# Kernel tuning notes

Hardware: AMD Instinct MI355X
Metric: run time of the kernel (lower is better)

The kernel has to match this reference:

```python
import jax, jax.numpy as jnp
import numpy as np

B, S, K, D, F, H, L, MLP = 8, 1024, 11, 512, 768, 8, 4, 2048
HD = D // H
LN_EPS = 1e-5
QK_EPS = 1e-6
SCALE = HD ** -0.5
W_STD = 0.02


def _ln(x, g, b):
    m = x.mean(-1, keepdims=True)
    v = ((x - m) ** 2).mean(-1, keepdims=True)
    return (x - m) / jnp.sqrt(v + LN_EPS) * g + b


def _lin(x, w, b):  # torch Linear: y = x @ W.T + b, W is [out, in]
    return jnp.einsum('...i,oi->...o', x, w) + b


def _heads(x):  # [b, t, D] -> [b, H, t, HD]
    b, t, _ = x.shape
    return x.reshape(b, t, H, HD).transpose(0, 2, 1, 3)


def _l2norm(x):  # F.normalize(dim=-1, eps=QK_EPS)
    n = jnp.sqrt((x * x).sum(-1, keepdims=True))
    return x / jnp.maximum(n, QK_EPS)


def _mha(xq, xkv, qw, qb, kw, kb, vw, vb, ow, ob, mask):
    q = _l2norm(_heads(_lin(xq, qw, qb)))
    k = _l2norm(_heads(_lin(xkv, kw, kb)))
    v = _heads(_lin(xkv, vw, vb))
    s = jnp.einsum('bhtd,bhsd->bhts', q, k) * SCALE
    if mask is not None:
        s = jnp.where(mask, jnp.finfo(s.dtype).min, s)
    a = jax.nn.softmax(s, axis=-1)
    c = jnp.einsum('bhts,bhsd->bhtd', a, v)
    c = c.transpose(0, 2, 1, 3).reshape(xq.shape[0], xq.shape[1], D)
    return _lin(c, ow, ob), a


def setup_inputs() -> dict:
    key = jax.random.key(0)
    ks = jax.random.split(key, 16)
    inp = {
        'features': jax.random.normal(ks[0], (B, S, F), jnp.float32),
        'slots': jax.random.normal(ks[1], (B, K, D), jnp.float32),
        'tok_w': jax.random.normal(ks[2], (D, F), jnp.float32) * W_STD,
        'tok_b': jnp.zeros((D,), jnp.float32),
        'slot_g': jnp.ones((D,), jnp.float32),
        'slot_b': jnp.zeros((D,), jnp.float32),
        'ln1_g': jnp.ones((L, D), jnp.float32),
        'ln1_b': jnp.zeros((L, D), jnp.float32),
        'ln2_g': jnp.ones((L, D), jnp.float32),
        'ln2_b': jnp.zeros((L, D), jnp.float32),
        'ln3_g': jnp.ones((L, D), jnp.float32),
        'ln3_b': jnp.zeros((L, D), jnp.float32),
    }
    names = ['sa_qw', 'sa_kw', 'sa_vw', 'sa_ow', 'ca_qw', 'ca_kw', 'ca_vw', 'ca_ow']
    for i, n in enumerate(names):
        inp[n] = jax.random.normal(ks[3 + i], (L, D, D), jnp.float32) * W_STD
        inp[n[:-1] + 'b'] = jnp.zeros((L, D), jnp.float32)
    inp['ffn_w1'] = jax.random.normal(ks[11], (L, MLP, D), jnp.float32) * W_STD
    inp['ffn_b1'] = jnp.zeros((L, MLP), jnp.float32)
    inp['ffn_w2'] = jax.random.normal(ks[12], (L, D, MLP), jnp.float32) * W_STD
    inp['ffn_b2'] = jnp.zeros((L, D), jnp.float32)
    return inp


def reference(features, slots, tok_w, tok_b, slot_g, slot_b,
              ln1_g, ln1_b, sa_qw, sa_qb, sa_kw, sa_kb, sa_vw, sa_vb, sa_ow, sa_ob,
              ln2_g, ln2_b, ca_qw, ca_qb, ca_kw, ca_kb, ca_vw, ca_vb, ca_ow, ca_ob,
              ln3_g, ln3_b, ffn_w1, ffn_b1, ffn_w2, ffn_b2):
    tokens = _lin(features, tok_w, tok_b)            # [B, S, D]
    slots_n = _ln(slots, slot_g, slot_b)             # [B, K, D]
    causal = jnp.triu(jnp.ones((S, S), bool), k=1)[None, None]  # True = masked
    cross_sum = jnp.zeros((B, S, K), tokens.dtype)
    for l in range(L):
        h = _ln(tokens, ln1_g[l], ln1_b[l])
        sa, _ = _mha(h, h, sa_qw[l], sa_qb[l], sa_kw[l], sa_kb[l],
                     sa_vw[l], sa_vb[l], sa_ow[l], sa_ob[l], causal)
        tokens = tokens + sa
        h = _ln(tokens, ln2_g[l], ln2_b[l])
        ca, w = _mha(h, slots_n, ca_qw[l], ca_qb[l], ca_kw[l], ca_kb[l],
                     ca_vw[l], ca_vb[l], ca_ow[l], ca_ob[l], None)
        tokens = tokens + ca
        cross_sum = cross_sum + w.mean(axis=1)       # avg over heads
        h = _ln(tokens, ln3_g[l], ln3_b[l])
        h = jax.nn.gelu(_lin(h, ffn_w1[l], ffn_b1[l]), approximate=False)
        tokens = tokens + _lin(h, ffn_w2[l], ffn_b2[l])
    masks = cross_sum / L                            # [B, S, K] avg over blocks
    return tokens, masks
```

## Files before the change

### kernel.cpp

```cpp
#include <hip/hip_runtime.h>
#include <math.h>

#define DEV __device__ __forceinline__

typedef __attribute__((ext_vector_type(4))) float f32x4;
typedef __attribute__((ext_vector_type(8))) short bf16x8;

DEV ushort f2bf(float x) {
  unsigned u = __float_as_uint(x);
  u = (u + 0x7FFFu + ((u >> 16) & 1u)) >> 16;
  return (ushort)u;
}

DEV float bf2f(ushort u) { return __uint_as_float(((unsigned)u) << 16); }

DEV ushort4 cvt4(float4 f) {
  ushort4 u;
  u.x = f2bf(f.x); u.y = f2bf(f.y); u.z = f2bf(f.z); u.w = f2bf(f.w);
  return u;
}

DEV float gelu_exact(float x) {
  return 0.5f * x * (1.0f + erff(x * 0.70710678118654752f));
}

DEV void async16(const void* g, void* l) {
  __builtin_amdgcn_global_load_lds((const __attribute__((address_space(1))) void*)g,
                                   (__attribute__((address_space(3))) void*)l, 16, 0, 0);
}

__global__ void prep_all(const float* __restrict__ features, const float* __restrict__ tok_w,
                         const float* __restrict__ sa_qw, const float* __restrict__ sa_kw,
                         const float* __restrict__ sa_vw, const float* __restrict__ sa_ow,
                         const float* __restrict__ ca_qw, const float* __restrict__ ca_kw,
                         const float* __restrict__ ca_vw, const float* __restrict__ ca_ow,
                         const float* __restrict__ ffn_w1, const float* __restrict__ ffn_w2,
                         const float* __restrict__ sa_qb, const float* __restrict__ sa_kb,
                         const float* __restrict__ sa_vb, const float* __restrict__ ca_kb,
                         const float* __restrict__ ca_vb,
                         ushort* __restrict__ featbf, ushort* __restrict__ tokwbf,
                         ushort* __restrict__ saowbf, ushort* __restrict__ caqwbf,
                         ushort* __restrict__ caowbf, ushort* __restrict__ w1bf,
                         ushort* __restrict__ w2bf, ushort* __restrict__ qkvwbf,
                         ushort* __restrict__ kvwbf, float* __restrict__ qkvb,
                         float* __restrict__ kvb) {
  long i = (long)blockIdx.x * 256 + threadIdx.x;
  if (i < 1572864) { ((ushort4*)featbf)[i] = cvt4(((const float4*)features)[i]); return; }
  i -= 1572864;
  if (i < 98304) { ((ushort4*)tokwbf)[i] = cvt4(((const float4*)tok_w)[i]); return; }
  i -= 98304;
  if (i < 262144) { ((ushort4*)saowbf)[i] = cvt4(((const float4*)sa_ow)[i]); return; }
  i -= 262144;
  if (i < 262144) { ((ushort4*)caqwbf)[i] = cvt4(((const float4*)ca_qw)[i]); return; }
  i -= 262144;
  if (i < 262144) { ((ushort4*)caowbf)[i] = cvt4(((const float4*)ca_ow)[i]); return; }
  i -= 262144;
  if (i < 1048576) { ((ushort4*)w1bf)[i] = cvt4(((const float4*)ffn_w1)[i]); return; }
  i -= 1048576;
  if (i < 1048576) { ((ushort4*)w2bf)[i] = cvt4(((const float4*)ffn_w2)[i]); return; }
  i -= 1048576;
  if (i < 786432) {
    const long o = i * 4;
    const int layer = (int)(o / 786432), r = (int)(o % 786432);
    const int sel = r / 262144, off = r % 262144;
    const float* s = (sel == 0 ? sa_qw : sel == 1 ? sa_kw : sa_vw) + (size_t)layer * 262144 + off;
    ((ushort4*)qkvwbf)[i] = cvt4(*(const float4*)s);
    return;
  }
  i -= 786432;
  if (i < 524288) {
    const long o = i * 4;
    const int layer = (int)(o / 524288), r = (int)(o % 524288);
    const int sel = r / 262144, off = r % 262144;
    const float* s = (sel == 0 ? ca_kw : ca_vw) + (size_t)layer * 262144 + off;
    ((ushort4*)kvwbf)[i] = cvt4(*(const float4*)s);
    return;
  }
  i -= 524288;
  if (i < 1536) {
    const long o = i * 4;
    const int layer = (int)(o / 1536), r = (int)(o % 1536);
    const int sel = r / 512, off = r % 512;
    const float* s = (sel == 0 ? sa_qb : sel == 1 ? sa_kb : sa_vb) + layer * 512 + off;
    ((float4*)qkvb)[i] = *(const float4*)s;
    return;
  }
  i -= 1536;
  if (i < 1024) {
    const long o = i * 4;
    const int layer = (int)(o / 1024), r = (int)(o % 1024);
    const int sel = r / 512, off = r % 512;
    const float* s = (sel == 0 ? ca_kb : ca_vb) + layer * 512 + off;
    ((float4*)kvb)[i] = *(const float4*)s;
  }
}

template <int EPI>
__launch_bounds__(256, 2)
__global__ void gemm_bt(const ushort* __restrict__ A, const ushort* __restrict__ W,
                        const float* __restrict__ bias, float* __restrict__ Yf,
                        ushort* __restrict__ Ybf, int M, int N, int K) {
  __shared__ ushort As[128 * 32];
  __shared__ ushort Bs[128 * 32];
  const int tid  = threadIdx.x;
  const int lane = tid & 63;
  const int wave = tid >> 6;
  const int wr = wave >> 1, wc = wave & 1;
  const int m0 = blockIdx.x * 128, n0 = blockIdx.y * 128;
  const int q = lane >> 4, ln = lane & 15;
  const int srow = lane >> 2;
  const int scol = (lane & 3) * 8;

  f32x4 acc[4][4] = {};

  const ushort* gA = A + (size_t)(m0 + wave * 32 + srow) * K + scol;
  const ushort* gB = W + (size_t)(n0 + wave * 32 + srow) * K + scol;
  ushort* lA = &As[(wave * 32) * 32];
  ushort* lB = &Bs[(wave * 32) * 32];

  for (int k0 = 0; k0 < K; k0 += 32) {
    async16(gA + k0, lA);
    async16(gA + k0 + (size_t)16 * K, lA + 16 * 32);
    async16(gB + k0, lB);
    async16(gB + k0 + (size_t)16 * K, lB + 16 * 32);
    __syncthreads();
    bf16x8 af[4], bfr[4];
#pragma unroll
    for (int t = 0; t < 4; ++t)
      af[t] = *(const bf16x8*)&As[(wr * 64 + t * 16 + ln) * 32 + q * 8];
#pragma unroll
    for (int t = 0; t < 4; ++t)
      bfr[t] = *(const bf16x8*)&Bs[(wc * 64 + t * 16 + ln) * 32 + q * 8];
#pragma unroll
    for (int mt = 0; mt < 4; ++mt)
#pragma unroll
      for (int nt = 0; nt < 4; ++nt)
        acc[mt][nt] = __builtin_amdgcn_mfma_f32_16x16x32_bf16(af[mt], bfr[nt], acc[mt][nt], 0, 0, 0);
    __syncthreads();
  }

  if (EPI >= 4) {
    const int chunk = (n0 + wc * 64) >> 9;
    const bool donorm = (EPI == 5 && chunk == 0) || (EPI == 6 && chunk < 2);
    const bool doscale = (EPI == 6 && chunk == 0);
#pragma unroll
    for (int mt = 0; mt < 4; ++mt) {
      const int gm = m0 + wr * 64 + mt * 16 + q * 4;
      float val[4][4];
#pragma unroll
      for (int nt = 0; nt < 4; ++nt) {
        const float bi = bias[n0 + wc * 64 + nt * 16 + ln];
#pragma unroll
        for (int r = 0; r < 4; ++r) val[nt][r] = acc[mt][nt][r] + bi;
      }
#pragma unroll
      for (int r = 0; r < 4; ++r) {
        float mult = 1.f;
        if (donorm) {
          float ss = val[0][r]*val[0][r] + val[1][r]*val[1][r] +
                     val[2][r]*val[2][r] + val[3][r]*val[3][r];
          ss += __shfl_xor(ss, 1);
          ss += __shfl_xor(ss, 2);
          ss += __shfl_xor(ss, 4);
          ss += __shfl_xor(ss, 8);
          mult = 1.f / fmaxf(sqrtf(ss), 1e-6f);
          if (doscale) mult *= 0.125f;
        }
#pragma unroll
        for (int nt = 0; nt < 4; ++nt) {
          const int gn = n0 + wc * 64 + nt * 16 + ln;
          Ybf[(size_t)(gm + r) * N + gn] = f2bf(val[nt][r] * mult);
        }
      }
    }
  } else {
#pragma unroll
    for (int mt = 0; mt < 4; ++mt) {
      const int gm = m0 + wr * 64 + mt * 16 + q * 4;
#pragma unroll
      for (int nt = 0; nt < 4; ++nt) {
        const int gn = n0 + wc * 64 + nt * 16 + ln;
        const float bi = bias[gn];
#pragma unroll
        for (int r = 0; r < 4; ++r) {
          const float val = acc[mt][nt][r] + bi;
          const size_t idx = (size_t)(gm + r) * N + gn;
          if (EPI == 0)      Yf[idx] = val;
          else if (EPI == 1) Yf[idx] += val;
          else               Ybf[idx] = f2bf(gelu_exact(val));
        }
      }
    }
  }
}

template <int EPI>
__launch_bounds__(256, 4)
__global__ void gemm_bt64(const ushort* __restrict__ A, const ushort* __restrict__ W,
                          const float* __restrict__ bias, float* __restrict__ Yf,
                          ushort* __restrict__ Ybf, int M, int N, int K) {
  __shared__ ushort As[64 * 32];
  __shared__ ushort Bs[64 * 32];
  __shared__ float red[2][32][2];
  const int tid = threadIdx.x, lane = tid & 63, wave = tid >> 6;
  const int wr = wave >> 1, wc = wave & 1;
  const int m0 = blockIdx.x * 64, n0 = blockIdx.y * 64;
  const int q = lane >> 4, ln = lane & 15;

  f32x4 acc[2][2] = {};
  const ushort* gA = A + (size_t)(m0 + wave * 16 + (lane >> 2)) * K + (lane & 3) * 8;
  const ushort* gB = W + (size_t)(n0 + wave * 16 + (lane >> 2)) * K + (lane & 3) * 8;
  ushort* lA = &As[wave * 16 * 32];
  ushort* lB = &Bs[wave * 16 * 32];

  for (int k0 = 0; k0 < K; k0 += 32) {
    async16(gA + k0, lA);
    async16(gB + k0, lB);
    __syncthreads();
    bf16x8 af[2], bfr[2];
#pragma unroll
    for (int t = 0; t < 2; ++t)
      af[t] = *(const bf16x8*)&As[(wr * 32 + t * 16 + ln) * 32 + q * 8];
#pragma unroll
    for (int t = 0; t < 2; ++t)
      bfr[t] = *(const bf16x8*)&Bs[(wc * 32 + t * 16 + ln) * 32 + q * 8];
#pragma unroll
    for (int mt = 0; mt < 2; ++mt)
#pragma unroll
      for (int nt = 0; nt < 2; ++nt)
        acc[mt][nt] = __builtin_amdgcn_mfma_f32_16x16x32_bf16(af[mt], bfr[nt], acc[mt][nt], 0, 0, 0);
    __syncthreads();
  }

  if (EPI == 4) {
    float val[2][2][4];
#pragma unroll
    for (int mt = 0; mt < 2; ++mt)
#pragma unroll
      for (int nt = 0; nt < 2; ++nt) {
        const float bi = bias[n0 + wc * 32 + nt * 16 + ln];
#pragma unroll
        for (int r = 0; r < 4; ++r) val[mt][nt][r] = acc[mt][nt][r] + bi;
      }
#pragma unroll
    for (int mt = 0; mt < 2; ++mt)
#pragma unroll
      for (int r = 0; r < 4; ++r) {
        float ss = val[mt][0][r]*val[mt][0][r] + val[mt][1][r]*val[mt][1][r];
        ss += __shfl_xor(ss, 1);
        ss += __shfl_xor(ss, 2);
        ss += __shfl_xor(ss, 4);
        ss += __shfl_xor(ss, 8);
        if (ln == 0) red[wr][mt * 16 + q * 4 + r][wc] = ss;
      }
    __syncthreads();
#pragma unroll
    for (int mt = 0; mt < 2; ++mt) {
      const int gm = m0 + wr * 32 + mt * 16 + q * 4;
#pragma unroll
      for (int r = 0; r < 4; ++r) {
        const float tot = red[wr][mt * 16 + q * 4 + r][0] + red[wr][mt * 16 + q * 4 + r][1];
        const float inv = 0.125f / fmaxf(sqrtf(tot), 1e-6f);
#pragma unroll
        for (int nt = 0; nt < 2; ++nt) {
          const int gn = n0 + wc * 32 + nt * 16 + ln;
          Ybf[(size_t)(gm + r) * N + gn] = f2bf(val[mt][nt][r] * inv);
        }
      }
    }
  } else {
#pragma unroll
    for (int mt = 0; mt < 2; ++mt) {
      const int gm = m0 + wr * 32 + mt * 16 + q * 4;
#pragma unroll
      for (int nt = 0; nt < 2; ++nt) {
        const int gn = n0 + wc * 32 + nt * 16 + ln;
        const float bi = bias[gn];
#pragma unroll
        for (int r = 0; r < 4; ++r) {
          const float val = acc[mt][nt][r] + bi;
          const size_t idx = (size_t)(gm + r) * N + gn;
          if (EPI == 0) Yf[idx] = val;
          else          Yf[idx] += val;
        }
      }
    }
  }
}

template <int BF>
__launch_bounds__(256)
__global__ void ln512(const float* __restrict__ X, const float* __restrict__ G,
                      const float* __restrict__ Bb, void* __restrict__ Yv, int rows) {
  const int lane = threadIdx.x & 63;
  const int wave = threadIdx.x >> 6;
  const int row = blockIdx.x * 4 + wave;
  if (row >= rows) return;
  const float* x = X + (size_t)row * 512 + lane * 8;
  float4 v0 = *(const float4*)x;
  float4 v1 = *(const float4*)(x + 4);
  float s = v0.x + v0.y + v0.z + v0.w + v1.x + v1.y + v1.z + v1.w;
#pragma unroll
  for (int off = 32; off; off >>= 1) s += __shfl_xor(s, off);
  const float mean = s * (1.f / 512.f);
  float d[8] = {v0.x - mean, v0.y - mean, v0.z - mean, v0.w - mean,
                v1.x - mean, v1.y - mean, v1.z - mean, v1.w - mean};
  float ss = d[0]*d[0] + d[1]*d[1] + d[2]*d[2] + d[3]*d[3] +
             d[4]*d[4] + d[5]*d[5] + d[6]*d[6] + d[7]*d[7];
#pragma unroll
  for (int off = 32; off; off >>= 1) ss += __shfl_xor(ss, off);
  const float rstd = rsqrtf(ss * (1.f / 512.f) + 1e-5f);
  const float* gp = G + lane * 8;
  const float* bp = Bb + lane * 8;
  float4 g0 = *(const float4*)gp, g1 = *(const float4*)(gp + 4);
  float4 b0 = *(const float4*)bp, b1 = *(const float4*)(bp + 4);
  float y[8];
  y[0] = d[0]*rstd*g0.x + b0.x; y[1] = d[1]*rstd*g0.y + b0.y;
  y[2] = d[2]*rstd*g0.z + b0.z; y[3] = d[3]*rstd*g0.w + b0.w;
  y[4] = d[4]*rstd*g1.x + b1.x; y[5] = d[5]*rstd*g1.y + b1.y;
  y[6] = d[6]*rstd*g1.z + b1.z; y[7] = d[7]*rstd*g1.w + b1.w;
  if (BF) {
    ushort* o = (ushort*)Yv + (size_t)row * 512 + lane * 8;
    ushort4 u0, u1;
    u0.x = f2bf(y[0]); u0.y = f2bf(y[1]); u0.z = f2bf(y[2]); u0.w = f2bf(y[3]);
    u1.x = f2bf(y[4]); u1.y = f2bf(y[5]); u1.z = f2bf(y[6]); u1.w = f2bf(y[7]);
    *(ushort4*)o = u0; *(ushort4*)(o + 4) = u1;
  } else {
    float* o = (float*)Yv + (size_t)row * 512 + lane * 8;
    *(float4*)o = make_float4(y[0], y[1], y[2], y[3]);
    *(float4*)(o + 4) = make_float4(y[4], y[5], y[6], y[7]);
  }
}

__launch_bounds__(256, 2)
__global__ void attn_self_mfma(const ushort* __restrict__ QKV, ushort* __restrict__ O) {
  constexpr int LDK = 72;
  __shared__ ushort Ks[64 * LDK];
  __shared__ ushort Vt[64 * LDK];
  __shared__ ushort Ps[4][32 * LDK];
  ushort* Qstage = &Ps[0][0];
  const int bi = blockIdx.x;
  const int half = bi >> 8, j = bi & 255;
  const int qt = half ? 7 - (j >> 5) : (j >> 5);
  const int bh = (half << 5) | (j & 31);
  const int b = bh >> 3, h = bh & 7;
  const size_t base = (size_t)b * 1024 * 1536 + h * 64;
  const int tid = threadIdx.x, lane = tid & 63, wave = tid >> 6;
  const int quad = lane >> 4, ln = lane & 15;

  const int kr = tid >> 2, kc0 = (tid & 3) * 16;
  const ushort* kbase = QKV + base + 512 + (size_t)kr * 1536 + kc0;
  const int vk = (tid & 31) * 2, vd0 = (tid >> 5) * 8;
  const ushort* vbase = QKV + base + 1024 + (size_t)vk * 1536 + vd0;

#pragma unroll
  for (int it = 0; it < 4; ++it) {
    const int idx = tid + 256 * it;
    const int r = idx >> 3, c = (idx & 7) * 8;
    *(uint4*)&Qstage[r * LDK + c] =
        *(const uint4*)(QKV + base + (size_t)(qt * 128 + r) * 1536 + c);
  }
  uint4 kreg0 = *(const uint4*)kbase;
  uint4 kreg1 = *(const uint4*)(kbase + 8);
  uint4 vreg0 = *(const uint4*)vbase;
  uint4 vreg1 = *(const uint4*)(vbase + 1536);
  __syncthreads();
  bf16x8 qf[2][2];
#pragma unroll
  for (int mt = 0; mt < 2; ++mt)
#pragma unroll
    for (int kc = 0; kc < 2; ++kc)
      qf[mt][kc] = *(const bf16x8*)&Qstage[(wave * 32 + mt * 16 + ln) * LDK + kc * 32 + quad * 8];

  float l_r[2][4] = {};
  f32x4 o_acc[2][4] = {};

  const int ktmax = 2 * qt + 1;
  for (int kt = 0; kt <= ktmax; ++kt) {
    __syncthreads();
    *(uint4*)&Ks[kr * LDK + kc0]     = kreg0;
    *(uint4*)&Ks[kr * LDK + kc0 + 8] = kreg1;
    {
      const ushort* ua = (const ushort*)&vreg0;
      const ushort* ub = (const ushort*)&vreg1;
#pragma unroll
      for (int jj = 0; jj < 8; ++jj)
        *(unsigned*)&Vt[(vd0 + jj) * LDK + vk] = (unsigned)ua[jj] | ((unsigned)ub[jj] << 16);
    }
    __syncthreads();
    if (kt < ktmax) {
      const size_t nb = (size_t)(kt + 1) * 64 * 1536;
      kreg0 = *(const uint4*)(kbase + nb);
      kreg1 = *(const uint4*)(kbase + nb + 8);
      vreg0 = *(const uint4*)(vbase + nb);
      vreg1 = *(const uint4*)(vbase + nb + 1536);
    }

    bf16x8 kf[4][2];
#pragma unroll
    for (int kb = 0; kb < 4; ++kb)
#pragma unroll
      for (int kc = 0; kc < 2; ++kc)
        kf[kb][kc] = *(const bf16x8*)&Ks[(kb * 16 + ln) * LDK + kc * 32 + quad * 8];
    f32x4 s[2][4] = {};
#pragma unroll
    for (int mt = 0; mt < 2; ++mt)
#pragma unroll
      for (int kb = 0; kb < 4; ++kb) {
        s[mt][kb] = __builtin_amdgcn_mfma_f32_16x16x32_bf16(qf[mt][0], kf[kb][0], s[mt][kb], 0, 0, 0);
        s[mt][kb] = __builtin_amdgcn_mfma_f32_16x16x32_bf16(qf[mt][1], kf[kb][1], s[mt][kb], 0, 0, 0);
      }

    const bool diag = (kt >= 2 * qt);
#pragma unroll
    for (int mt = 0; mt < 2; ++mt) {
      const int qrow0 = qt * 128 + wave * 32 + mt * 16 + quad * 4;
#pragma unroll
      for (int kb = 0; kb < 4; ++kb) {
        const int kcol = kt * 64 + kb * 16 + ln;
#pragma unroll
        for (int r = 0; r < 4; ++r) {
          float p = __expf(s[mt][kb][r]);
          if (diag && kcol > qrow0 + r) p = 0.f;
          l_r[mt][r] += p;
          Ps[wave][(mt * 16 + quad * 4 + r) * LDK + kb * 16 + ln] = f2bf(p);
        }
      }
    }
    __builtin_amdgcn_wave_barrier();

    bf16x8 pf[2][2];
#pragma unroll
    for (int mt = 0; mt < 2; ++mt)
#pragma unroll
      for (int kc = 0; kc < 2; ++kc)
        pf[mt][kc] = *(const bf16x8*)&Ps[wave][(mt * 16 + ln) * LDK + kc * 32 + quad * 8];
#pragma unroll
    for (int db = 0; db < 4; ++db) {
      bf16x8 vf0 = *(const bf16x8*)&Vt[(db * 16 + ln) * LDK + quad * 8];
      bf16x8 vf1 = *(const bf16x8*)&Vt[(db * 16 + ln) * LDK + 32 + quad * 8];
#pragma unroll
      for (int mt = 0; mt < 2; ++mt) {
        o_acc[mt][db] = __builtin_amdgcn_mfma_f32_16x16x32_bf16(pf[mt][0], vf0, o_acc[mt][db], 0, 0, 0);
        o_acc[mt][db] = __builtin_amdgcn_mfma_f32_16x16x32_bf16(pf[mt][1], vf1, o_acc[mt][db], 0, 0, 0);
      }
    }
  }

  const size_t obase = (size_t)b * 1024 * 512 + h * 64;
#pragma unroll
  for (int mt = 0; mt < 2; ++mt) {
    const int qrow0 = qt * 128 + wave * 32 + mt * 16 + quad * 4;
#pragma unroll
    for (int r = 0; r < 4; ++r) {
      float l = l_r[mt][r];
      l += __shfl_xor(l, 1);
      l += __shfl_xor(l, 2);
      l += __shfl_xor(l, 4);
      l += __shfl_xor(l, 8);
      const float inv = 1.f / l;
      ushort* dst = O + obase + (size_t)(qrow0 + r) * 512;
#pragma unroll
      for (int db = 0; db < 4; ++db)
        dst[db * 16 + ln] = f2bf(o_acc[mt][db][r] * inv);
    }
  }
}

__launch_bounds__(128)
__global__ void attn_cross(const ushort* __restrict__ Q, const ushort* __restrict__ KV,
                           ushort* __restrict__ Obf, float* __restrict__ mask_out) {
  const int rt = blockIdx.x;
  const int bh = blockIdx.y;
  const int b = bh >> 3, h = bh & 7;
  const int tid = threadIdx.x;
  __shared__ float Qs[128][65];
  __shared__ float Kcs[11][64];
  __shared__ float Vcs[11][64];
  const size_t base = ((size_t)(b * 1024)) * 512 + h * 64;

  for (int i = tid; i < 704; i += 128) {
    const int k = i >> 6, d = i & 63;
    Kcs[k][d] = bf2f(KV[((size_t)(b * 11 + k)) * 1024 + h * 64 + d]);
    Vcs[k][d] = bf2f(KV[((size_t)(b * 11 + k)) * 1024 + 512 + h * 64 + d]);
  }
#pragma unroll
  for (int it = 0; it < 8; ++it) {
    const int idx = tid + 128 * it;
    const int r = idx >> 3, c = (idx & 7) * 8;
    uint4 t = *(const uint4*)(Q + base + (size_t)(rt * 128 + r) * 512 + c);
    const ushort* u = (const ushort*)&t;
#pragma unroll
    for (int jj = 0; jj < 8; ++jj) Qs[r][c + jj] = bf2f(u[jj]);
  }
  __syncthreads();

  float s[11] = {};
  for (int d = 0; d < 64; ++d) {
    const float qv = Qs[tid][d];
#pragma unroll
    for (int k = 0; k < 11; ++k) s[k] += qv * Kcs[k][d];
  }
  float l = 0.f;
#pragma unroll
  for (int k = 0; k < 11; ++k) { s[k] = __expf(s[k]); l += s[k]; }
  const float inv = 1.f / l;
#pragma unroll
  for (int k = 0; k < 11; ++k) s[k] *= inv;

  const int qrow = rt * 128 + tid;
  float* mo = mask_out + ((size_t)(b * 1024 + qrow)) * 11;
#pragma unroll
  for (int k = 0; k < 11; ++k) atomicAdd(mo + k, s[k] * 0.03125f);

  ushort* dst = Obf + base + (size_t)qrow * 512;
#pragma unroll
  for (int d0 = 0; d0 < 64; d0 += 8) {
    ushort o8[8];
#pragma unroll
    for (int jj = 0; jj < 8; ++jj) {
      float acc = 0.f;
#pragma unroll
      for (int k = 0; k < 11; ++k) acc += s[k] * Vcs[k][d0 + jj];
      o8[jj] = f2bf(acc);
    }
    *(uint4*)(dst + d0) = *(const uint4*)o8;
  }
}

extern "C" void kernel_launch(void* const* d_in, const int* in_sizes, int n_in,
                              void* d_out, int out_size, void* d_ws, size_t ws_size,
                              hipStream_t stream) {
  const float* features = (const float*)d_in[0];
  const float* slots    = (const float*)d_in[1];
  const float* tok_w    = (const float*)d_in[2];
  const float* tok_b    = (const float*)d_in[3];
  const float* slot_g   = (const float*)d_in[4];
  const float* slot_b   = (const float*)d_in[5];
  const float* ln1_g    = (const float*)d_in[6];
  const float* ln1_b    = (const float*)d_in[7];
  const float* ln2_g    = (const float*)d_in[8];
  const float* ln2_b    = (const float*)d_in[9];
  const float* ln3_g    = (const float*)d_in[10];
  const float* ln3_b    = (const float*)d_in[11];
  const float* sa_qw = (const float*)d_in[12]; const float* sa_qb = (const float*)d_in[13];
  const float* sa_kw = (const float*)d_in[14]; const float* sa_kb = (const float*)d_in[15];
  const float* sa_vw = (const float*)d_in[16]; const float* sa_vb = (const float*)d_in[17];
  const float* sa_ow = (const float*)d_in[18]; const float* sa_ob = (const float*)d_in[19];
  const float* ca_qw = (const float*)d_in[20]; const float* ca_qb = (const float*)d_in[21];
  const float* ca_kw = (const float*)d_in[22]; const float* ca_kb = (const float*)d_in[23];
  const float* ca_vw = (const float*)d_in[24]; const float* ca_vb = (const float*)d_in[25];
  const float* ca_ow = (const float*)d_in[26]; const float* ca_ob = (const float*)d_in[27];
  const float* ffn_w1 = (const float*)d_in[28]; const float* ffn_b1 = (const float*)d_in[29];
  const float* ffn_w2 = (const float*)d_in[30]; const float* ffn_b2 = (const float*)d_in[31];

  float* tokens = (float*)d_out;
  float* masks  = (float*)d_out + 4194304;

  char* wp = (char*)d_ws;
  size_t off = 0;
  auto carve = [&](size_t bytes) -> void* {
    void* p = wp + off;
    off = (off + bytes + 255) & ~(size_t)255;
    return p;
  };
  ushort* hbf     = (ushort*)carve(8192ull * 512 * 2);
  ushort* qkvbf   = (ushort*)carve(8192ull * 1536 * 2);
  ushort* qbf     = (ushort*)carve(8192ull * 512 * 2);
  ushort* cbf     = (ushort*)carve(8192ull * 512 * 2);
  ushort* hidbf   = (ushort*)carve(8192ull * 2048 * 2);
  ushort* slotsn  = (ushort*)carve(128ull * 512 * 2);
  ushort* kvc     = (ushort*)carve(128ull * 1024 * 2);
  ushort* tokwbf  = (ushort*)carve(512ull * 768 * 2);
  ushort* saowbf  = (ushort*)carve(4ull * 512 * 512 * 2);
  ushort* caqwbf  = (ushort*)carve(4ull * 512 * 512 * 2);
  ushort* caowbf  = (ushort*)carve(4ull * 512 * 512 * 2);
  ushort* w1bf    = (ushort*)carve(4ull * 2048 * 512 * 2);
  ushort* w2bf    = (ushort*)carve(4ull * 512 * 2048 * 2);
  ushort* qkvwbf  = (ushort*)carve(4ull * 1536 * 512 * 2);
  ushort* kvwbf   = (ushort*)carve(4ull * 1024 * 512 * 2);
  float*  qkvb    = (float*)carve(4ull * 1536 * 4);
  float*  kvb     = (float*)carve(4ull * 1024 * 4);
  ushort* featbf  = hidbf;

  prep_all<<<22922, 256, 0, stream>>>(features, tok_w, sa_qw, sa_kw, sa_vw, sa_ow,
                                      ca_qw, ca_kw, ca_vw, ca_ow, ffn_w1, ffn_w2,
                                      sa_qb, sa_kb, sa_vb, ca_kb, ca_vb,
                                      featbf, tokwbf, saowbf, caqwbf, caowbf,
                                      w1bf, w2bf, qkvwbf, kvwbf, qkvb, kvb);
  hipMemsetAsync(masks, 0, 90112ull * 4, stream);

  gemm_bt64<0><<<dim3(128, 8), 256, 0, stream>>>(featbf, tokwbf, tok_b, tokens, (ushort*)nullptr, 8192, 512, 768);
  ln512<1><<<22, 256, 0, stream>>>(slots, slot_g, slot_b, slotsn, 88);

  for (int l = 0; l < 4; ++l) {
    const size_t wD = (size_t)l * 512 * 512;
    const size_t bD = (size_t)l * 512;
    ln512<1><<<2048, 256, 0, stream>>>(tokens, ln1_g + bD, ln1_b + bD, hbf, 8192);
    gemm_bt<6><<<dim3(64, 12), 256, 0, stream>>>(hbf, qkvwbf + (size_t)l * 1536 * 512, qkvb + l * 1536,
                                                 (float*)nullptr, qkvbf, 8192, 1536, 512);
    attn_self_mfma<<<512, 256, 0, stream>>>(qkvbf, cbf);
    gemm_bt64<1><<<dim3(128, 8), 256, 0, stream>>>(cbf, saowbf + wD, sa_ob + bD, tokens, (ushort*)nullptr, 8192, 512, 512);
    ln512<1><<<2048, 256, 0, stream>>>(tokens, ln2_g + bD, ln2_b + bD, hbf, 8192);
    gemm_bt64<4><<<dim3(128, 8), 256, 0, stream>>>(hbf, caqwbf + wD, ca_qb + bD, (float*)nullptr, qbf, 8192, 512, 512);
    gemm_bt<5><<<dim3(1, 8), 256, 0, stream>>>(slotsn, kvwbf + (size_t)l * 1024 * 512, kvb + l * 1024,
                                               (float*)nullptr, kvc, 128, 1024, 512);
    attn_cross<<<dim3(8, 64), 128, 0, stream>>>(qbf, kvc, cbf, masks);
    gemm_bt64<1><<<dim3(128, 8), 256, 0, stream>>>(cbf, caowbf + wD, ca_ob + bD, tokens, (ushort*)nullptr, 8192, 512, 512);
    const size_t wM = (size_t)l * 2048 * 512;
    const size_t bM = (size_t)l * 2048;
    ln512<1><<<2048, 256, 0, stream>>>(tokens, ln3_g + bD, ln3_b + bD, hbf, 8192);
    gemm_bt<2><<<dim3(64, 16), 256, 0, stream>>>(hbf, w1bf + wM, ffn_b1 + bM, (float*)nullptr, hidbf, 8192, 2048, 512);
    gemm_bt64<1><<<dim3(128, 8), 256, 0, stream>>>(hidbf, w2bf + wM, ffn_b2 + bD, tokens, (ushort*)nullptr, 8192, 512, 2048);
  }
}
```

Baseline: 1.136 ms.

## Split cross-attention rows across 8 lanes and fold mask zeroing into prep

The cross-attention kernel now gives each query row to 8 threads, each covering 8 head dims, and combines the partial dot products with lane shuffles. This removes the shared-memory Q staging and the per-thread 64-long serial loop, raises the grid to 32x64 blocks of 256 threads, and spreads the mask atomics and output writes across lanes. The hipMemsetAsync for masks is replaced by extra threads in prep_all, saving one launch. In exchange the kernel performs more shuffles and the K/V staging is repeated per block, since there are more blocks.

Result: faster. 1.023 ms (-9.9%).

```diff
diff --git a/kernel.cpp b/kernel.cpp
--- a/kernel.cpp
+++ b/kernel.cpp
@@ -43,7 +43,7 @@
                          ushort* __restrict__ caowbf, ushort* __restrict__ w1bf,
                          ushort* __restrict__ w2bf, ushort* __restrict__ qkvwbf,
                          ushort* __restrict__ kvwbf, float* __restrict__ qkvb,
-                         float* __restrict__ kvb) {
+                         float* __restrict__ kvb, float* __restrict__ masks) {
   long i = (long)blockIdx.x * 256 + threadIdx.x;
   if (i < 1572864) { ((ushort4*)featbf)[i] = cvt4(((const float4*)features)[i]); return; }
   i -= 1572864;
@@ -92,6 +92,11 @@
     const int sel = r / 512, off = r % 512;
     const float* s = (sel == 0 ? ca_kb : ca_vb) + layer * 512 + off;
     ((float4*)kvb)[i] = *(const float4*)s;
+    return;
+  }
+  i -= 1024;
+  if (i < 22528) {
+    ((float4*)masks)[i] = make_float4(0.f, 0.f, 0.f, 0.f);
   }
 }
 
@@ -467,39 +472,45 @@
   }
 }
 
-__launch_bounds__(128)
+__launch_bounds__(256)
 __global__ void attn_cross(const ushort* __restrict__ Q, const ushort* __restrict__ KV,
                            ushort* __restrict__ Obf, float* __restrict__ mask_out) {
   const int rt = blockIdx.x;
   const int bh = blockIdx.y;
   const int b = bh >> 3, h = bh & 7;
   const int tid = threadIdx.x;
-  __shared__ float Qs[128][65];
   __shared__ float Kcs[11][64];
   __shared__ float Vcs[11][64];
   const size_t base = ((size_t)(b * 1024)) * 512 + h * 64;
 
-  for (int i = tid; i < 704; i += 128) {
+  for (int i = tid; i < 704; i += 256) {
     const int k = i >> 6, d = i & 63;
     Kcs[k][d] = bf2f(KV[((size_t)(b * 11 + k)) * 1024 + h * 64 + d]);
     Vcs[k][d] = bf2f(KV[((size_t)(b * 11 + k)) * 1024 + 512 + h * 64 + d]);
   }
-#pragma unroll
-  for (int it = 0; it < 8; ++it) {
-    const int idx = tid + 128 * it;
-    const int r = idx >> 3, c = (idx & 7) * 8;
-    uint4 t = *(const uint4*)(Q + base + (size_t)(rt * 128 + r) * 512 + c);
-    const ushort* u = (const ushort*)&t;
-#pragma unroll
-    for (int jj = 0; jj < 8; ++jj) Qs[r][c + jj] = bf2f(u[jj]);
-  }
   __syncthreads();
 
-  float s[11] = {};
-  for (int d = 0; d < 64; ++d) {
-    const float qv = Qs[tid][d];
-#pragma unroll
-    for (int k = 0; k < 11; ++k) s[k] += qv * Kcs[k][d];
+  const int g = tid >> 3;
+  const int lj = tid & 7;
+  const int qrow = rt * 32 + g;
+  const int d0 = lj * 8;
+
+  uint4 qv4 = *(const uint4*)(Q + base + (size_t)qrow * 512 + d0);
+  const ushort* qu = (const ushort*)&qv4;
+  float qv[8];
+#pragma unroll
+  for (int jj = 0; jj < 8; ++jj) qv[jj] = bf2f(qu[jj]);
+
+  float s[11];
+#pragma unroll
+  for (int k = 0; k < 11; ++k) {
+    float acc = 0.f;
+#pragma unroll
+    for (int jj = 0; jj < 8; ++jj) acc += qv[jj] * Kcs[k][d0 + jj];
+    acc += __shfl_xor(acc, 1);
+    acc += __shfl_xor(acc, 2);
+    acc += __shfl_xor(acc, 4);
+    s[k] = acc;
   }
   float l = 0.f;
 #pragma unroll
@@ -508,24 +519,19 @@
 #pragma unroll
   for (int k = 0; k < 11; ++k) s[k] *= inv;
 
-  const int qrow = rt * 128 + tid;
   float* mo = mask_out + ((size_t)(b * 1024 + qrow)) * 11;
-#pragma unroll
-  for (int k = 0; k < 11; ++k) atomicAdd(mo + k, s[k] * 0.03125f);
-
-  ushort* dst = Obf + base + (size_t)qrow * 512;
-#pragma unroll
-  for (int d0 = 0; d0 < 64; d0 += 8) {
-    ushort o8[8];
-#pragma unroll
-    for (int jj = 0; jj < 8; ++jj) {
-      float acc = 0.f;
-#pragma unroll
-      for (int k = 0; k < 11; ++k) acc += s[k] * Vcs[k][d0 + jj];
-      o8[jj] = f2bf(acc);
-    }
-    *(uint4*)(dst + d0) = *(const uint4*)o8;
-  }
+  atomicAdd(mo + lj, s[lj] * 0.03125f);
+  if (lj < 3) atomicAdd(mo + lj + 8, s[lj + 8] * 0.03125f);
+
+  ushort o8[8];
+#pragma unroll
+  for (int jj = 0; jj < 8; ++jj) {
+    float acc = 0.f;
+#pragma unroll
+    for (int k = 0; k < 11; ++k) acc += s[k] * Vcs[k][d0 + jj];
+    o8[jj] = f2bf(acc);
+  }
+  *(uint4*)(Obf + base + (size_t)qrow * 512 + d0) = *(const uint4*)o8;
 }
 
 extern "C" void kernel_launch(void* const* d_in, const int* in_sizes, int n_in,
@@ -583,12 +589,11 @@
   float*  kvb     = (float*)carve(4ull * 1024 * 4);
   ushort* featbf  = hidbf;
 
-  prep_all<<<22922, 256, 0, stream>>>(features, tok_w, sa_qw, sa_kw, sa_vw, sa_ow,
+  prep_all<<<23010, 256, 0, stream>>>(features, tok_w, sa_qw, sa_kw, sa_vw, sa_ow,
                                       ca_qw, ca_kw, ca_vw, ca_ow, ffn_w1, ffn_w2,
                                       sa_qb, sa_kb, sa_vb, ca_kb, ca_vb,
                                       featbf, tokwbf, saowbf, caqwbf, caowbf,
-                                      w1bf, w2bf, qkvwbf, kvwbf, qkvb, kvb);
-  hipMemsetAsync(masks, 0, 90112ull * 4, stream);
+                                      w1bf, w2bf, qkvwbf, kvwbf, qkvb, kvb, masks);
 
   gemm_bt64<0><<<dim3(128, 8), 256, 0, stream>>>(featbf, tokwbf, tok_b, tokens, (ushort*)nullptr, 8192, 512, 768);
   ln512<1><<<22, 256, 0, stream>>>(slots, slot_g, slot_b, slotsn, 88);
@@ -605,7 +610,7 @@
     gemm_bt64<4><<<dim3(128, 8), 256, 0, stream>>>(hbf, caqwbf + wD, ca_qb + bD, (float*)nullptr, qbf, 8192, 512, 512);
     gemm_bt<5><<<dim3(1, 8), 256, 0, stream>>>(slotsn, kvwbf + (size_t)l * 1024 * 512, kvb + l * 1024,
                                                (float*)nullptr, kvc, 128, 1024, 512);
-    attn_cross<<<dim3(8, 64), 128, 0, stream>>>(qbf, kvc, cbf, masks);
+    attn_cross<<<dim3(32, 64), 256, 0, stream>>>(qbf, kvc, cbf, masks);
     gemm_bt64<1><<<dim3(128, 8), 256, 0, stream>>>(cbf, caowbf + wD, ca_ob + bD, tokens, (ushort*)nullptr, 8192, 512, 512);
     const size_t wM = (size_t)l * 2048 * 512;
     const size_t bM = (size_t)l * 2048;
```
